# Kernel optimization log

Measured on AMD Instinct MI355X. Metric: run time of the kernel, lower is better.

The kernel has to match this reference:

```python
import jax, jax.numpy as jnp
import numpy as np

# ---- dims ----
N_NODES = 33      # nodes per graph (33-bus grid)
SEQ     = 24      # time steps per sample
BATCH   = 64      # samples
G       = BATCH * SEQ          # total graphs in the batch
EPG     = 64                   # directed edges per graph
E       = G * EPG              # total edges
N       = G * N_NODES          # total nodes
IN_CH   = 2
HID     = 64
HEADS   = 8
HC      = HID * HEADS          # 512
EDGE_DIM = 3
LSTM1_H = 128
LSTM2_H = 64
N_CLASSES = 4
NEG_SLOPE = 0.2


def setup_inputs() -> dict:
    key = jax.random.key(0)
    ks = jax.random.split(key, 32)
    rng = np.random.default_rng(0)

    # block-structured edge_index: every edge stays inside its own graph
    off = np.repeat(np.arange(G, dtype=np.int64) * N_NODES, EPG)
    src = rng.integers(0, N_NODES, E) + off
    dst = rng.integers(0, N_NODES, E) + off
    edge_index = jnp.asarray(np.stack([src, dst]), dtype=jnp.int32)

    def glorot(k, shape):
        fan = shape[0] + shape[-1]
        s = jnp.sqrt(6.0 / fan).astype(jnp.float32)
        return jax.random.uniform(k, shape, jnp.float32, -s, s)

    inp = dict(
        x=jax.random.normal(ks[0], (N, IN_CH), jnp.float32),
        edge_index=edge_index,
        edge_attr=jax.random.uniform(ks[1], (E, EDGE_DIM), jnp.float32),
        # GATv2 layer 1 (concat=True)
        g1_Wl=glorot(ks[2], (IN_CH, HC)),
        g1_Wr=glorot(ks[3], (IN_CH, HC)),
        g1_We=glorot(ks[4], (EDGE_DIM, HC)),
        g1_att=glorot(ks[5], (HEADS, HID)),
        g1_b=jnp.zeros((HC,), jnp.float32),
        # GATv2 layer 2 (concat=False -> head mean)
        g2_Wl=glorot(ks[6], (HC, HC)),
        g2_Wr=glorot(ks[7], (HC, HC)),
        g2_We=glorot(ks[8], (EDGE_DIM, HC)),
        g2_att=glorot(ks[9], (HEADS, HID)),
        g2_b=jnp.zeros((HID,), jnp.float32),
        # LSTM1: input 33*64=2112 -> 128, gates ordered (i,f,g,o)
        l1_Wih=0.05 * jax.random.normal(ks[10], (4 * LSTM1_H, N_NODES * HID), jnp.float32),
        l1_Whh=0.05 * jax.random.normal(ks[11], (4 * LSTM1_H, LSTM1_H), jnp.float32),
        l1_bih=jnp.zeros((4 * LSTM1_H,), jnp.float32),
        l1_bhh=jnp.zeros((4 * LSTM1_H,), jnp.float32),
        # LSTM2: 128 -> 64
        l2_Wih=0.05 * jax.random.normal(ks[12], (4 * LSTM2_H, LSTM1_H), jnp.float32),
        l2_Whh=0.05 * jax.random.normal(ks[13], (4 * LSTM2_H, LSTM2_H), jnp.float32),
        l2_bih=jnp.zeros((4 * LSTM2_H,), jnp.float32),
        l2_bhh=jnp.zeros((4 * LSTM2_H,), jnp.float32),
        # FC 64 -> n_classes
        fc_W=0.05 * jax.random.normal(ks[14], (N_CLASSES, LSTM2_H), jnp.float32),
        fc_b=jnp.zeros((N_CLASSES,), jnp.float32),
    )
    return inp


def _gatv2(x, edge_attr, src, dst, Wl, Wr, We, att, b, concat):
    """PyG GATv2Conv with edge_dim, add_self_loops semantics omitted is NOT used:
    we follow the message math: m = leaky_relu(xl[src]+xr[dst]+We@e),
    alpha = segment_softmax(<m,att>, dst), out = scatter_add(alpha * xl[src])."""
    n = x.shape[0]
    xl = (x @ Wl).reshape(n, HEADS, HID)      # [N,H,C]
    xr = (x @ Wr).reshape(n, HEADS, HID)
    em = (edge_attr @ We).reshape(-1, HEADS, HID)  # [E,H,C]
    m = jax.nn.leaky_relu(xl[src] + xr[dst] + em, NEG_SLOPE)
    logits = jnp.einsum('ehc,hc->eh', m, att)          # [E,H]
    mx = jax.ops.segment_max(logits, dst, num_segments=n)   # [N,H]
    ex = jnp.exp(logits - mx[dst])
    den = jax.ops.segment_sum(ex, dst, num_segments=n)
    alpha = ex / (den[dst] + 1e-16)                    # [E,H]
    out = jax.ops.segment_sum(xl[src] * alpha[:, :, None], dst, num_segments=n)  # [N,H,C]
    out = out.reshape(n, HC) if concat else out.mean(axis=1)
    return out + b


def _lstm(x, Wih, Whh, bih, bhh, hsz):
    B = x.shape[0]
    h0 = jnp.zeros((B, hsz), x.dtype)
    c0 = jnp.zeros((B, hsz), x.dtype)

    def step(carry, xt):
        h, c = carry
        gates = xt @ Wih.T + h @ Whh.T + bih + bhh
        i, f, g, o = jnp.split(gates, 4, axis=-1)
        i = jax.nn.sigmoid(i); f = jax.nn.sigmoid(f)
        g = jnp.tanh(g);       o = jax.nn.sigmoid(o)
        c = f * c + i * g
        h = o * jnp.tanh(c)
        return (h, c), h

    _, ys = jax.lax.scan(step, (h0, c0), x.transpose(1, 0, 2))  # [T,B,H]
    return ys.transpose(1, 0, 2)


def reference(x, edge_index, edge_attr,
              g1_Wl, g1_Wr, g1_We, g1_att, g1_b,
              g2_Wl, g2_Wr, g2_We, g2_att, g2_b,
              l1_Wih, l1_Whh, l1_bih, l1_bhh,
              l2_Wih, l2_Whh, l2_bih, l2_bhh,
              fc_W, fc_b):
    src, dst = edge_index[0], edge_index[1]
    h = jax.nn.elu(_gatv2(x, edge_attr, src, dst, g1_Wl, g1_Wr, g1_We, g1_att, g1_b, True))
    h = jax.nn.elu(_gatv2(h, edge_attr, src, dst, g2_Wl, g2_Wr, g2_We, g2_att, g2_b, False))
    seq = h.reshape(BATCH, SEQ, N_NODES * HID)          # [B,T,2112]
    seq = _lstm(seq, l1_Wih, l1_Whh, l1_bih, l1_bhh, LSTM1_H)
    seq = _lstm(seq, l2_Wih, l2_Whh, l2_bih, l2_bhh, LSTM2_H)
    last = seq[:, -1, :]                                 # [B,64]
    return last @ fc_W.T + fc_b                          # [B,n_classes]
```

## Files before the change

kernel.cpp:

```cpp
#include <hip/hip_runtime.h>
#include <math.h>

#define N_NODES 33
#define SEQ 24
#define BATCH 64
#define G_GRAPHS (BATCH * SEQ)
#define EPG 64
#define E_EDGES (G_GRAPHS * EPG)
#define N_TOTAL (G_GRAPHS * N_NODES)
#define HID 64
#define HEADS 8
#define HC (HID * HEADS)
#define LSTM1_H 128
#define LSTM2_H 64
#define NEG_SLOPE 0.2f
#define CONV_BLOCKS (128 + 264)

__device__ __forceinline__ float sigmoidf_(float x) { return 1.f / (1.f + expf(-x)); }
__device__ __forceinline__ float eluf_(float x) { return x > 0.f ? x : expm1f(x); }
__device__ __forceinline__ float lreluf_(float x) { return x > 0.f ? x : NEG_SLOPE * x; }

typedef __attribute__((ext_vector_type(4))) float f32x4;
typedef _Float16 half_t;
typedef __attribute__((ext_vector_type(8))) _Float16 halfx8;

__device__ __forceinline__ void gl2lds16(const void* g, void* l) {
  __builtin_amdgcn_global_load_lds(
      (__attribute__((address_space(1))) const unsigned int*)g,
      (__attribute__((address_space(3))) unsigned int*)l, 16, 0, 0);
}

__global__ __launch_bounds__(512) void gat1_kernel(
    const float* __restrict__ x, const int* __restrict__ src, const int* __restrict__ dst,
    const float* __restrict__ ea, const float* __restrict__ Wl, const float* __restrict__ Wr,
    const float* __restrict__ We, const float* __restrict__ att, const float* __restrict__ bias,
    half_t* __restrict__ h1, int g0, int gat_blocks,
    const float* __restrict__ g2Wl, const float* __restrict__ g2Wr,
    half_t* __restrict__ B2, const float* __restrict__ W1, half_t* __restrict__ W1f) {
  const int tid = threadIdx.x;

  __shared__ alignas(16) float Wl_s[2 * 512];
  __shared__ alignas(16) float Wr_s[2 * 512];
  __shared__ alignas(16) float We_s[3 * 512];
  __shared__ alignas(16) float att_s[512];
  __shared__ float xs0_s[N_NODES + 1], xs1_s[N_NODES + 1];
  __shared__ float easX[EPG], easY[EPG], easZ[EPG];
  __shared__ float logit_s[HEADS * 65];
  __shared__ int sloc[EPG], dloc[EPG], deg[N_NODES], start[N_NODES], fill[N_NODES], elist[EPG];
  __shared__ float tr[64 * 65];

  if ((int)blockIdx.x >= gat_blocks) {
    int cb = blockIdx.x - gat_blocks;
    if (cb < 128) {
      int kt = cb & 7, nt = cb >> 3;
      int k0 = kt * 64, n0 = nt * 64;
      int r = tid >> 6, c = tid & 63;
      #pragma unroll
      for (int rr = 0; rr < 8; ++rr) {
        int kl = rr * 8 + r;
        int n = n0 + c;
        float v = (n < 512) ? g2Wl[(size_t)(k0 + kl) * 512 + n]
                            : g2Wr[(size_t)(k0 + kl) * 512 + n - 512];
        tr[kl * 65 + c] = v;
      }
      __syncthreads();
      #pragma unroll
      for (int rr = 0; rr < 8; ++rr) {
        int nl = rr * 8 + r;
        B2[(size_t)(n0 + nl) * 512 + k0 + c] = (half_t)tr[c * 65 + nl];
      }
    } else {
      int base = (cb - 128) * 4096 + tid;
      #pragma unroll
      for (int i = 0; i < 8; ++i) {
        int idx = base + i * 512;
        if (idx < 512 * 2112) W1f[idx] = (half_t)W1[idx];
      }
    }
    return;
  }

  const int g = g0 + blockIdx.x;
  const int nb = g * N_NODES, eb = g * EPG;
  const int lb = blockIdx.x * N_NODES;

  for (int i = tid; i < 1024; i += 512) { Wl_s[i] = Wl[i]; Wr_s[i] = Wr[i]; }
  for (int i = tid; i < 1536; i += 512) We_s[i] = We[i];
  if (tid < 512) att_s[tid] = att[tid];
  if (tid < 2 * N_NODES) {
    float v = x[nb * 2 + tid];
    if (tid & 1) xs1_s[tid >> 1] = v; else xs0_s[tid >> 1] = v;
  }
  if (tid < EPG) {
    easX[tid] = ea[(eb + tid) * 3 + 0];
    easY[tid] = ea[(eb + tid) * 3 + 1];
    easZ[tid] = ea[(eb + tid) * 3 + 2];
    sloc[tid] = src[eb + tid] - nb;
    dloc[tid] = dst[eb + tid] - nb;
  }
  if (tid < N_NODES) { deg[tid] = 0; fill[tid] = 0; }
  __syncthreads();
  if (tid < EPG) atomicAdd(&deg[dloc[tid]], 1);
  __syncthreads();
  if (tid == 0) { int a = 0; for (int n = 0; n < N_NODES; ++n) { start[n] = a; a += deg[n]; } }
  __syncthreads();
  if (tid < EPG) { int d = dloc[tid]; int p = atomicAdd(&fill[d], 1); elist[start[d] + p] = tid; }

  {
    int h = tid >> 6, e = tid & 63;
    int s = sloc[e], d = dloc[e];
    float xs0 = xs0_s[s], xs1 = xs1_s[s], xd0 = xs0_s[d], xd1 = xs1_s[d];
    float e0 = easX[e], e1 = easY[e], e2 = easZ[e];
    float acc = 0.f;
    int base = h * 64;
    #pragma unroll
    for (int c4 = 0; c4 < 16; ++c4) {
      int j = base + c4 * 4;
      f32x4 wl0 = *(const f32x4*)(Wl_s + j);
      f32x4 wl1 = *(const f32x4*)(Wl_s + 512 + j);
      f32x4 wr0 = *(const f32x4*)(Wr_s + j);
      f32x4 wr1 = *(const f32x4*)(Wr_s + 512 + j);
      f32x4 we0 = *(const f32x4*)(We_s + j);
      f32x4 we1 = *(const f32x4*)(We_s + 512 + j);
      f32x4 we2 = *(const f32x4*)(We_s + 1024 + j);
      f32x4 at  = *(const f32x4*)(att_s + j);
      #pragma unroll
      for (int q = 0; q < 4; ++q) {
        float v = xs0 * wl0[q] + xs1 * wl1[q]
                + xd0 * wr0[q] + xd1 * wr1[q]
                + e0 * we0[q] + e1 * we1[q] + e2 * we2[q];
        acc += lreluf_(v) * at[q];
      }
    }
    logit_s[h * 65 + e] = acc;
  }
  __syncthreads();

  {
    int h = tid >> 6, n = tid & 63;
    if (n < N_NODES) {
      int s0 = start[n], dn = deg[n];
      float mx = -1e30f;
      for (int i = 0; i < dn; ++i) mx = fmaxf(mx, logit_s[h * 65 + elist[s0 + i]]);
      float den = 0.f;
      for (int i = 0; i < dn; ++i) den += expf(logit_s[h * 65 + elist[s0 + i]] - mx);
      float inv = 1.f / (den + 1e-16f);
      for (int i = 0; i < dn; ++i) {
        int e = elist[s0 + i];
        logit_s[h * 65 + e] = expf(logit_s[h * 65 + e] - mx) * inv;
      }
    }
  }
  __syncthreads();

  for (int t = tid; t < N_NODES * 64; t += 512) {
    int n = t >> 6, jb = t & 63;
    int j0 = jb * 8, h = jb >> 3;
    f32x4 wa0 = *(const f32x4*)(Wl_s + j0);
    f32x4 wa1 = *(const f32x4*)(Wl_s + j0 + 4);
    f32x4 wb0 = *(const f32x4*)(Wl_s + 512 + j0);
    f32x4 wb1 = *(const f32x4*)(Wl_s + 512 + j0 + 4);
    float acc[8] = {};
    int s0 = start[n], dn = deg[n];
    for (int i = 0; i < dn; ++i) {
      int e = elist[s0 + i]; int s = sloc[e];
      float a = logit_s[h * 65 + e];
      float ax0 = a * xs0_s[s], ax1 = a * xs1_s[s];
      #pragma unroll
      for (int q = 0; q < 4; ++q) {
        acc[q]     += ax0 * wa0[q] + ax1 * wb0[q];
        acc[4 + q] += ax0 * wa1[q] + ax1 * wb1[q];
      }
    }
    f32x4 b0 = *(const f32x4*)(bias + j0);
    f32x4 b1 = *(const f32x4*)(bias + j0 + 4);
    halfx8 vh;
    #pragma unroll
    for (int cc = 0; cc < 8; ++cc) {
      float bb = (cc < 4) ? b0[cc] : b1[cc - 4];
      vh[cc] = (half_t)eluf_(acc[cc] + bb);
    }
    *(halfx8*)(h1 + (size_t)(lb + n) * HC + j0) = vh;
  }
}

template <int WM, int WN, int NP, int K, int SA, int SB, typename TC>
__global__ __launch_bounds__(256) void gemm_f16(
    const half_t* __restrict__ A, const half_t* __restrict__ B,
    TC* __restrict__ C, const float* __restrict__ bias1, const float* __restrict__ bias2,
    int M, int N) {
  constexpr int BM = 32 * WM, BN = 32 * WN;
  constexpr bool BOUNCE = (sizeof(TC) == 2) && (BM == 128) && (BN == 128);
  constexpr int STAGE_HALFS = (BM + BN) * 32 * NP;
  constexpr int CT_HALFS = BOUNCE ? 128 * 132 : 0;
  constexpr int LDS_HALFS = STAGE_HALFS > CT_HALFS ? STAGE_HALFS : CT_HALFS;
  __shared__ half_t lds[LDS_HALFS];
  half_t* A_s = lds;
  half_t* B_s = A_s + NP * BM * 32;

  const int R = M / BM, NT = N / BN;
  int b = blockIdx.x;
  int xcd = b & 7, q = b >> 3;
  int ct = q % NT, rg = q / NT;
  int r = rg * 8 + xcd;
  if (r >= R) return;

  const int tid = threadIdx.x;
  const int wave = tid >> 6, lane = tid & 63;
  const int wm = wave >> 1, wn = wave & 1;
  const int bm = r * BM, bn = ct * BN;

  const int rA = lane >> 2;
  const int swz = (rA & 3) ^ ((rA >> 2) & 3);
  const int cA = ((lane & 3) ^ swz) * 8;

  f32x4 acc[WM][WN];
  #pragma unroll
  for (int tm = 0; tm < WM; ++tm)
    #pragma unroll
    for (int tn = 0; tn < WN; ++tn) acc[tm][tn] = {0.f, 0.f, 0.f, 0.f};

  for (int k0 = 0; k0 < K; k0 += 32 * NP) {
    #pragma unroll
    for (int p = 0; p < NP; ++p) {
      int kk = k0 + p * 32;
      #pragma unroll
      for (int i = 0; i < BM / 64; ++i) {
        int row = i * 64 + wave * 16;
        gl2lds16(A + (size_t)(bm + row + rA) * SA + kk + cA,
                 A_s + p * BM * 32 + row * 32);
      }
      #pragma unroll
      for (int i = 0; i < BN / 64; ++i) {
        int row = i * 64 + wave * 16;
        gl2lds16(B + (size_t)(bn + row + rA) * SB + kk + cA,
                 B_s + p * BN * 32 + row * 32);
      }
    }
    __syncthreads();

    const int fr = lane & 15;
    const int fs = (fr & 3) ^ ((fr >> 2) & 3);
    const int fk = ((lane >> 4) ^ fs) * 8;
    #pragma unroll
    for (int p = 0; p < NP; ++p) {
      const int pA = p * BM * 32, pB = p * BN * 32;
      halfx8 af[WM], bf[WN];
      #pragma unroll
      for (int tm = 0; tm < WM; ++tm) {
        int rr = (wm * WM + tm) * 16 + fr;
        af[tm] = *(const halfx8*)(A_s + pA + rr * 32 + fk);
      }
      #pragma unroll
      for (int tn = 0; tn < WN; ++tn) {
        int rr = (wn * WN + tn) * 16 + fr;
        bf[tn] = *(const halfx8*)(B_s + pB + rr * 32 + fk);
      }
      #pragma unroll
      for (int tm = 0; tm < WM; ++tm)
        #pragma unroll
        for (int tn = 0; tn < WN; ++tn)
          acc[tm][tn] = __builtin_amdgcn_mfma_f32_16x16x32_f16(af[tm], bf[tn], acc[tm][tn], 0, 0, 0);
    }
    __syncthreads();
  }

  const int col0 = lane & 15, rq = (lane >> 4) * 4;
  if constexpr (BOUNCE) {
    half_t* Cs = lds;
    #pragma unroll
    for (int tm = 0; tm < WM; ++tm)
      #pragma unroll
      for (int tn = 0; tn < WN; ++tn) {
        int cl = (wn * WN + tn) * 16 + col0;
        #pragma unroll
        for (int rr = 0; rr < 4; ++rr) {
          int rl = (wm * WM + tm) * 16 + rq + rr;
          Cs[rl * 132 + cl] = (half_t)acc[tm][tn][rr];
        }
      }
    __syncthreads();
    #pragma unroll
    for (int pass = 0; pass < 8; ++pass) {
      int row = pass * 16 + (tid >> 4);
      int col = (tid & 15) * 8;
      halfx8 v = *(const halfx8*)(Cs + row * 132 + col);
      *(halfx8*)((half_t*)C + (size_t)(bm + row) * N + bn + col) = v;
    }
  } else {
    #pragma unroll
    for (int tm = 0; tm < WM; ++tm)
      #pragma unroll
      for (int tn = 0; tn < WN; ++tn) {
        int col = bn + (wn * WN + tn) * 16 + col0;
        float badd = 0.f;
        if (bias1) badd += bias1[col];
        if (bias2) badd += bias2[col];
        #pragma unroll
        for (int rr = 0; rr < 4; ++rr) {
          int row = bm + (wm * WM + tm) * 16 + rq + rr;
          C[(size_t)row * N + col] = (TC)(acc[tm][tn][rr] + badd);
        }
      }
  }
}

__global__ __launch_bounds__(256) void gemm_f16_splitk(
    const half_t* __restrict__ A, const half_t* __restrict__ B,
    float* __restrict__ Cp, const float* __restrict__ bias1, const float* __restrict__ bias2,
    int M, int N) {
  constexpr int SA = 2112;
  __shared__ half_t lds[(64 + 64) * 64];
  half_t* A_s = lds;
  half_t* B_s = A_s + 2 * 64 * 32;

  const int part = blockIdx.y;
  const int koff = part ? 576 + (part - 1) * 512 : 0;
  const int kend = part ? 512 : 576;
  const half_t* Ap = A + koff;
  const half_t* Bp = B + koff;
  float* C = Cp + (size_t)part * M * N;

  const int R = M / 64, NT = N / 64;
  int b = blockIdx.x;
  int xcd = b & 7, q = b >> 3;
  int ct = q % NT, rg = q / NT;
  int r = rg * 8 + xcd;
  if (r >= R) return;

  const int tid = threadIdx.x;
  const int wave = tid >> 6, lane = tid & 63;
  const int wm = wave >> 1, wn = wave & 1;
  const int bm = r * 64, bn = ct * 64;

  const int rA = lane >> 2;
  const int swz = (rA & 3) ^ ((rA >> 2) & 3);
  const int cA = ((lane & 3) ^ swz) * 8;

  f32x4 acc[2][2];
  #pragma unroll
  for (int tm = 0; tm < 2; ++tm)
    #pragma unroll
    for (int tn = 0; tn < 2; ++tn) acc[tm][tn] = {0.f, 0.f, 0.f, 0.f};

  for (int k0 = 0; k0 < kend; k0 += 64) {
    #pragma unroll
    for (int p = 0; p < 2; ++p) {
      int kk = k0 + p * 32;
      int row = wave * 16;
      gl2lds16(Ap + (size_t)(bm + row + rA) * SA + kk + cA,
               A_s + p * 64 * 32 + row * 32);
      gl2lds16(Bp + (size_t)(bn + row + rA) * SA + kk + cA,
               B_s + p * 64 * 32 + row * 32);
    }
    __syncthreads();
    const int fr = lane & 15;
    const int fs = (fr & 3) ^ ((fr >> 2) & 3);
    const int fk = ((lane >> 4) ^ fs) * 8;
    #pragma unroll
    for (int p = 0; p < 2; ++p) {
      const int pA = p * 64 * 32, pB = p * 64 * 32;
      halfx8 af[2], bf[2];
      #pragma unroll
      for (int tm = 0; tm < 2; ++tm) {
        int rr = (wm * 2 + tm) * 16 + fr;
        af[tm] = *(const halfx8*)(A_s + pA + rr * 32 + fk);
      }
      #pragma unroll
      for (int tn = 0; tn < 2; ++tn) {
        int rr = (wn * 2 + tn) * 16 + fr;
        bf[tn] = *(const halfx8*)(B_s + pB + rr * 32 + fk);
      }
      #pragma unroll
      for (int tm = 0; tm < 2; ++tm)
        #pragma unroll
        for (int tn = 0; tn < 2; ++tn)
          acc[tm][tn] = __builtin_amdgcn_mfma_f32_16x16x32_f16(af[tm], bf[tn], acc[tm][tn], 0, 0, 0);
    }
    __syncthreads();
  }

  const int col0 = lane & 15, rq = (lane >> 4) * 4;
  #pragma unroll
  for (int tm = 0; tm < 2; ++tm)
    #pragma unroll
    for (int tn = 0; tn < 2; ++tn) {
      int col = bn + (wn * 2 + tn) * 16 + col0;
      float badd = (part == 0) ? (bias1[col] + bias2[col]) : 0.f;
      #pragma unroll
      for (int rr = 0; rr < 4; ++rr) {
        int row = bm + (wm * 2 + tm) * 16 + rq + rr;
        C[(size_t)row * N + col] = acc[tm][tn][rr] + badd;
      }
    }
}

__global__ __launch_bounds__(512) void gat2_kernel(
    const half_t* __restrict__ xlr, const int* __restrict__ src, const int* __restrict__ dst,
    const float* __restrict__ ea, const float* __restrict__ We,
    const float* __restrict__ att, const float* __restrict__ bias,
    half_t* __restrict__ h2, int g0) {
  __shared__ alignas(16) float We_s[3 * 512];
  __shared__ alignas(16) float att_s[512];
  __shared__ float b_s[HID];
  __shared__ float easX[EPG], easY[EPG], easZ[EPG];
  __shared__ float logit_s[HEADS * 65];
  __shared__ int sloc[EPG], dloc[EPG], deg[N_NODES], start[N_NODES], fill[N_NODES], elist[EPG];

  const int g = g0 + blockIdx.x, tid = threadIdx.x;
  const int nb = g * N_NODES, eb = g * EPG;
  const int lb = blockIdx.x * N_NODES;
  const int wave = tid >> 6, lane = tid & 63;

  for (int i = tid; i < 1536; i += 512) We_s[i] = We[i];
  if (tid < 512) att_s[tid] = att[tid];
  if (tid < HID) b_s[tid] = bias[tid];
  if (tid < EPG) {
    easX[tid] = ea[(eb + tid) * 3 + 0];
    easY[tid] = ea[(eb + tid) * 3 + 1];
    easZ[tid] = ea[(eb + tid) * 3 + 2];
    sloc[tid] = src[eb + tid] - nb;
    dloc[tid] = dst[eb + tid] - nb;
  }
  if (tid < N_NODES) { deg[tid] = 0; fill[tid] = 0; }
  __syncthreads();
  if (tid < EPG) atomicAdd(&deg[dloc[tid]], 1);
  __syncthreads();
  if (tid == 0) { int a = 0; for (int n = 0; n < N_NODES; ++n) { start[n] = a; a += deg[n]; } }
  __syncthreads();
  if (tid < EPG) { int d = dloc[tid]; int p = atomicAdd(&fill[d], 1); elist[start[d] + p] = tid; }
  __syncthreads();

  const int j0 = lane * 8;
  float w0[8], w1[8], w2[8], at8[8];
  #pragma unroll
  for (int q = 0; q < 8; ++q) {
    w0[q] = We_s[j0 + q];
    w1[q] = We_s[512 + j0 + q];
    w2[q] = We_s[1024 + j0 + q];
    at8[q] = att_s[j0 + q];
  }

  for (int e = wave; e < EPG; e += 8) {
    int s = sloc[e], d = dloc[e];
    halfx8 xlv = *((const halfx8*)(xlr + (size_t)(lb + s) * 1024) + lane);
    halfx8 xrv = *((const halfx8*)(xlr + (size_t)(lb + d) * 1024 + 512) + lane);
    float e0 = easX[e], e1 = easY[e], e2 = easZ[e];
    float acc = 0.f;
    #pragma unroll
    for (int q = 0; q < 8; ++q) {
      float v = (float)xlv[q] + (float)xrv[q] + e0 * w0[q] + e1 * w1[q] + e2 * w2[q];
      acc += lreluf_(v) * at8[q];
    }
    acc += __shfl_xor(acc, 1, 64);
    acc += __shfl_xor(acc, 2, 64);
    acc += __shfl_xor(acc, 4, 64);
    if ((lane & 7) == 0) logit_s[(lane >> 3) * 65 + e] = acc;
  }
  __syncthreads();

  {
    int h = tid >> 6, n = tid & 63;
    if (n < N_NODES) {
      int s0 = start[n], dn = deg[n];
      float mx = -1e30f;
      for (int i = 0; i < dn; ++i) mx = fmaxf(mx, logit_s[h * 65 + elist[s0 + i]]);
      float den = 0.f;
      for (int i = 0; i < dn; ++i) den += expf(logit_s[h * 65 + elist[s0 + i]] - mx);
      float inv = 1.f / (den + 1e-16f);
      for (int i = 0; i < dn; ++i) {
        int e = elist[s0 + i];
        logit_s[h * 65 + e] = expf(logit_s[h * 65 + e] - mx) * inv;
      }
    }
  }
  __syncthreads();

  for (int n = wave; n < N_NODES; n += 8) {
    float acc = 0.f;
    int s0 = start[n], dn = deg[n];
    for (int i = 0; i < dn; ++i) {
      int e = elist[s0 + i], s = sloc[e];
      const half_t* row = xlr + (size_t)(lb + s) * 1024 + lane;
      #pragma unroll
      for (int h = 0; h < 8; ++h)
        acc += logit_s[h * 65 + e] * (float)row[h * 64];
    }
    float v = eluf_(acc * 0.125f + b_s[lane]);
    h2[(size_t)(nb + n) * HID + lane] = (half_t)v;
  }
}

__global__ __launch_bounds__(1024, 4) void lstm_all(
    const float* __restrict__ X0, const float* __restrict__ X1,
    const float* __restrict__ X2p, const float* __restrict__ X3,
    const float* __restrict__ Whh1,
    const float* __restrict__ Wih2, const float* __restrict__ bih2,
    const float* __restrict__ bhh2, const float* __restrict__ Whh2,
    const float* __restrict__ fcW, const float* __restrict__ fcb,
    float* __restrict__ out) {
  __shared__ float hs1[LSTM1_H], cs1[LSTM1_H], p1[512], gs1[512];
  __shared__ float Y1s[SEQ][LSTM1_H];
  __shared__ float hs2[LSTM2_H], cs2[LSTM2_H], p2[4 * 256], gs2[256];
  const int tid = threadIdx.x, b = blockIdx.x;
  const int j = tid & 511, half = tid >> 9;

  float4 w1[16];
  {
    const float4* wp = (const float4*)(Whh1 + (size_t)j * LSTM1_H + half * 64);
    #pragma unroll
    for (int q = 0; q < 16; ++q) w1[q] = wp[q];
  }
  if (tid < LSTM1_H) { hs1[tid] = 0.f; cs1[tid] = 0.f; }
  __syncthreads();
  for (int t = 0; t < SEQ; ++t) {
    const float* hb = hs1 + half * 64;
    float acc = 0.f;
    #pragma unroll
    for (int q = 0; q < 16; ++q) {
      acc += w1[q].x * hb[4 * q] + w1[q].y * hb[4 * q + 1]
           + w1[q].z * hb[4 * q + 2] + w1[q].w * hb[4 * q + 3];
    }
    if (half) p1[j] = acc;
    __syncthreads();
    if (!half) {
      size_t xo = ((size_t)b * SEQ + t) * 512 + j;
      gs1[j] = acc + p1[j] + X0[xo] + X1[xo] + X2p[xo] + X3[xo];
    }
    __syncthreads();
    if (tid < LSTM1_H) {
      float ig = sigmoidf_(gs1[tid]);
      float fg = sigmoidf_(gs1[LSTM1_H + tid]);
      float gg = tanhf(gs1[2 * LSTM1_H + tid]);
      float og = sigmoidf_(gs1[3 * LSTM1_H + tid]);
      float c = fg * cs1[tid] + ig * gg;
      cs1[tid] = c;
      float h = og * tanhf(c);
      hs1[tid] = h;
      Y1s[t][tid] = h;
    }
    __syncthreads();
  }

  const int j2 = tid & 255, qt = tid >> 8;
  float4 w2x[8], w2h[4];
  {
    const float4* wxp = (const float4*)(Wih2 + (size_t)j2 * LSTM1_H + qt * 32);
    #pragma unroll
    for (int q = 0; q < 8; ++q) w2x[q] = wxp[q];
    const float4* whp = (const float4*)(Whh2 + (size_t)j2 * LSTM2_H + qt * 16);
    #pragma unroll
    for (int q = 0; q < 4; ++q) w2h[q] = whp[q];
  }
  if (tid < LSTM2_H) { hs2[tid] = 0.f; cs2[tid] = 0.f; }
  __syncthreads();
  for (int t = 0; t < SEQ; ++t) {
    const float* y = Y1s[t] + qt * 32;
    const float* hb = hs2 + qt * 16;
    float acc = 0.f;
    #pragma unroll
    for (int q = 0; q < 8; ++q) {
      acc += w2x[q].x * y[4 * q] + w2x[q].y * y[4 * q + 1]
           + w2x[q].z * y[4 * q + 2] + w2x[q].w * y[4 * q + 3];
    }
    #pragma unroll
    for (int q = 0; q < 4; ++q) {
      acc += w2h[q].x * hb[4 * q] + w2h[q].y * hb[4 * q + 1]
           + w2h[q].z * hb[4 * q + 2] + w2h[q].w * hb[4 * q + 3];
    }
    p2[qt * 256 + j2] = acc;
    __syncthreads();
    if (qt == 0)
      gs2[j2] = p2[j2] + p2[256 + j2] + p2[512 + j2] + p2[768 + j2]
              + bih2[j2] + bhh2[j2];
    __syncthreads();
    if (tid < LSTM2_H) {
      float ig = sigmoidf_(gs2[tid]);
      float fg = sigmoidf_(gs2[LSTM2_H + tid]);
      float gg = tanhf(gs2[2 * LSTM2_H + tid]);
      float og = sigmoidf_(gs2[3 * LSTM2_H + tid]);
      float c = fg * cs2[tid] + ig * gg;
      cs2[tid] = c;
      hs2[tid] = og * tanhf(c);
    }
    __syncthreads();
  }
  if (tid < 4) {
    float acc = fcb[tid];
    #pragma unroll
    for (int k = 0; k < LSTM2_H; ++k) acc += fcW[tid * LSTM2_H + k] * hs2[k];
    out[b * 4 + tid] = acc;
  }
}

extern "C" void kernel_launch(void* const* d_in, const int* in_sizes, int n_in,
                              void* d_out, int out_size, void* d_ws, size_t ws_size,
                              hipStream_t stream) {
  const float* x       = (const float*)d_in[0];
  const int*   eidx    = (const int*)d_in[1];
  const float* eattr   = (const float*)d_in[2];
  const float* g1_Wl   = (const float*)d_in[3];
  const float* g1_Wr   = (const float*)d_in[4];
  const float* g1_We   = (const float*)d_in[5];
  const float* g1_att  = (const float*)d_in[6];
  const float* g1_b    = (const float*)d_in[7];
  const float* g2_Wl   = (const float*)d_in[8];
  const float* g2_Wr   = (const float*)d_in[9];
  const float* g2_We   = (const float*)d_in[10];
  const float* g2_att  = (const float*)d_in[11];
  const float* g2_b    = (const float*)d_in[12];
  const float* l1_Wih  = (const float*)d_in[13];
  const float* l1_Whh  = (const float*)d_in[14];
  const float* l1_bih  = (const float*)d_in[15];
  const float* l1_bhh  = (const float*)d_in[16];
  const float* l2_Wih  = (const float*)d_in[17];
  const float* l2_Whh  = (const float*)d_in[18];
  const float* l2_bih  = (const float*)d_in[19];
  const float* l2_bhh  = (const float*)d_in[20];
  const float* fc_W    = (const float*)d_in[21];
  const float* fc_b    = (const float*)d_in[22];
  float* out = (float*)d_out;

  const int* src = eidx;
  const int* dst = eidx + E_EDGES;

  const int cand[5] = {1, 2, 3, 4, 6};
  int nchunks = 0;
  half_t *h1 = nullptr, *xlr2c = nullptr, *h2 = nullptr, *B2 = nullptr, *W1f = nullptr;
  float *X1p = nullptr;
  int chunk_g = 0, chunk_n = 0;
  for (int ci = 0; ci < 5; ++ci) {
    int C = cand[ci];
    int CG = G_GRAPHS / C, CN = CG * N_NODES;
    char* p = (char*)d_ws;
    auto alloc = [&](size_t bytes) { char* r = p; p += (bytes + 255) & ~(size_t)255; return r; };
    half_t* t_h1    = (half_t*)alloc((size_t)CN * HC * 2);
    half_t* t_xlr2c = (half_t*)alloc((size_t)CN * 1024 * 2);
    half_t* t_h2    = (half_t*)alloc((size_t)G_GRAPHS * 2112 * 2);
    half_t* t_B2    = (half_t*)alloc((size_t)1024 * 512 * 2);
    half_t* t_W1f   = (half_t*)alloc((size_t)512 * 2112 * 2);
    float*  t_X1p   = (float*)alloc((size_t)4 * G_GRAPHS * 512 * 4);
    if ((size_t)(p - (char*)d_ws) <= ws_size) {
      nchunks = C; chunk_g = CG; chunk_n = CN;
      h1 = t_h1; xlr2c = t_xlr2c; h2 = t_h2; B2 = t_B2; W1f = t_W1f;
      X1p = t_X1p;
      break;
    }
  }
  if (nchunks == 0) return;

  for (int c = 0; c < nchunks; ++c) {
    int g0 = c * chunk_g;
    int extra = (c == 0) ? CONV_BLOCKS : 0;
    gat1_kernel<<<chunk_g + extra, 512, 0, stream>>>(
        x, src, dst, eattr, g1_Wl, g1_Wr, g1_We, g1_att, g1_b, h1, g0, chunk_g,
        g2_Wl, g2_Wr, B2, l1_Wih, W1f);
    int R = chunk_n / 128, NT = 1024 / 128;
    int gblocks = 8 * ((R + 7) / 8) * NT;
    gemm_f16<4, 4, 2, HC, HC, HC, half_t><<<gblocks, 256, 0, stream>>>(
        h1, B2, xlr2c, (const float*)nullptr, (const float*)nullptr,
        chunk_n, 1024);
    gat2_kernel<<<chunk_g, 512, 0, stream>>>(xlr2c, src, dst, eattr, g2_We,
                                             g2_att, g2_b, h2, g0);
  }

  {
    dim3 grid(192, 4);
    gemm_f16_splitk<<<grid, 256, 0, stream>>>(h2, W1f, X1p, l1_bih, l1_bhh,
                                              G_GRAPHS, 512);
  }

  {
    size_t PS = (size_t)G_GRAPHS * 512;
    lstm_all<<<BATCH, 1024, 0, stream>>>(X1p, X1p + PS, X1p + 2 * PS, X1p + 3 * PS,
                                         l1_Whh, l2_Wih, l2_bih, l2_bhh, l2_Whh,
                                         fc_W, fc_b, out);
  }
}
```

Baseline: 344.7 us.

## Stage GAT2 node rows in LDS and drop a barrier per LSTM step

The GAT layer-2 kernel now copies each graph's 33 node rows (xl and xr halves) into shared memory with direct global-to-LDS loads. Edge logits and aggregation then read from LDS instead of re-gathering rows from global memory. Separately, both LSTM recurrences fold the partial-sum reduction into the gate-activation threads, removing one __syncthreads per time step, and the layer-2 bias is preloaded into a register. The staging adds about 66 KB of LDS per block, which lowers occupancy, and there is no visible wait or barrier between the async LDS copy and its first use.

```diff
diff --git a/kernel.cpp b/kernel.cpp
--- a/kernel.cpp
+++ b/kernel.cpp
@@ -400,6 +400,7 @@
     const float* __restrict__ ea, const float* __restrict__ We,
     const float* __restrict__ att, const float* __restrict__ bias,
     half_t* __restrict__ h2, int g0) {
+  __shared__ half_t x_s[N_NODES * 1024];
   __shared__ alignas(16) float We_s[3 * 512];
   __shared__ alignas(16) float att_s[512];
   __shared__ float b_s[HID];
@@ -411,6 +412,12 @@
   const int nb = g * N_NODES, eb = g * EPG;
   const int lb = blockIdx.x * N_NODES;
   const int wave = tid >> 6, lane = tid & 63;
+
+  for (int n = wave; n < N_NODES; n += 8) {
+    const half_t* grow = xlr + (size_t)(lb + n) * 1024;
+    gl2lds16(grow + lane * 8, x_s + n * 1024);
+    gl2lds16(grow + 512 + lane * 8, x_s + n * 1024 + 512);
+  }
 
   for (int i = tid; i < 1536; i += 512) We_s[i] = We[i];
   if (tid < 512) att_s[tid] = att[tid];
@@ -443,8 +450,8 @@
 
   for (int e = wave; e < EPG; e += 8) {
     int s = sloc[e], d = dloc[e];
-    halfx8 xlv = *((const halfx8*)(xlr + (size_t)(lb + s) * 1024) + lane);
-    halfx8 xrv = *((const halfx8*)(xlr + (size_t)(lb + d) * 1024 + 512) + lane);
+    halfx8 xlv = *((const halfx8*)(x_s + s * 1024) + lane);
+    halfx8 xrv = *((const halfx8*)(x_s + d * 1024 + 512) + lane);
     float e0 = easX[e], e1 = easY[e], e2 = easZ[e];
     float acc = 0.f;
     #pragma unroll
@@ -481,7 +488,7 @@
     int s0 = start[n], dn = deg[n];
     for (int i = 0; i < dn; ++i) {
       int e = elist[s0 + i], s = sloc[e];
-      const half_t* row = xlr + (size_t)(lb + s) * 1024 + lane;
+      const half_t* row = x_s + s * 1024 + lane;
       #pragma unroll
       for (int h = 0; h < 8; ++h)
         acc += logit_s[h * 65 + e] * (float)row[h * 64];
@@ -499,9 +506,9 @@
     const float* __restrict__ bhh2, const float* __restrict__ Whh2,
     const float* __restrict__ fcW, const float* __restrict__ fcb,
     float* __restrict__ out) {
-  __shared__ float hs1[LSTM1_H], cs1[LSTM1_H], p1[512], gs1[512];
+  __shared__ float hs1[LSTM1_H], cs1[LSTM1_H], p1[2][512];
   __shared__ float Y1s[SEQ][LSTM1_H];
-  __shared__ float hs2[LSTM2_H], cs2[LSTM2_H], p2[4 * 256], gs2[256];
+  __shared__ float hs2[LSTM2_H], cs2[LSTM2_H], p2[4][256];
   const int tid = threadIdx.x, b = blockIdx.x;
   const int j = tid & 511, half = tid >> 9;
 
@@ -521,19 +528,22 @@
       acc += w1[q].x * hb[4 * q] + w1[q].y * hb[4 * q + 1]
            + w1[q].z * hb[4 * q + 2] + w1[q].w * hb[4 * q + 3];
     }
-    if (half) p1[j] = acc;
-    __syncthreads();
     if (!half) {
       size_t xo = ((size_t)b * SEQ + t) * 512 + j;
-      gs1[j] = acc + p1[j] + X0[xo] + X1[xo] + X2p[xo] + X3[xo];
-    }
+      acc += X0[xo] + X1[xo] + X2p[xo] + X3[xo];
+    }
+    p1[half][j] = acc;
     __syncthreads();
     if (tid < LSTM1_H) {
-      float ig = sigmoidf_(gs1[tid]);
-      float fg = sigmoidf_(gs1[LSTM1_H + tid]);
-      float gg = tanhf(gs1[2 * LSTM1_H + tid]);
-      float og = sigmoidf_(gs1[3 * LSTM1_H + tid]);
-      float c = fg * cs1[tid] + ig * gg;
+      float gi = p1[0][tid] + p1[1][tid];
+      float gf = p1[0][LSTM1_H + tid] + p1[1][LSTM1_H + tid];
+      float gg = p1[0][2 * LSTM1_H + tid] + p1[1][2 * LSTM1_H + tid];
+      float go = p1[0][3 * LSTM1_H + tid] + p1[1][3 * LSTM1_H + tid];
+      float ig = sigmoidf_(gi);
+      float fg = sigmoidf_(gf);
+      float gv = tanhf(gg);
+      float og = sigmoidf_(go);
+      float c = fg * cs1[tid] + ig * gv;
       cs1[tid] = c;
       float h = og * tanhf(c);
       hs1[tid] = h;
@@ -544,6 +554,7 @@
 
   const int j2 = tid & 255, qt = tid >> 8;
   float4 w2x[8], w2h[4];
+  float bsum = 0.f;
   {
     const float4* wxp = (const float4*)(Wih2 + (size_t)j2 * LSTM1_H + qt * 32);
     #pragma unroll
@@ -551,13 +562,14 @@
     const float4* whp = (const float4*)(Whh2 + (size_t)j2 * LSTM2_H + qt * 16);
     #pragma unroll
     for (int q = 0; q < 4; ++q) w2h[q] = whp[q];
+    if (qt == 0) bsum = bih2[j2] + bhh2[j2];
   }
   if (tid < LSTM2_H) { hs2[tid] = 0.f; cs2[tid] = 0.f; }
   __syncthreads();
   for (int t = 0; t < SEQ; ++t) {
     const float* y = Y1s[t] + qt * 32;
     const float* hb = hs2 + qt * 16;
-    float acc = 0.f;
+    float acc = (qt == 0) ? bsum : 0.f;
     #pragma unroll
     for (int q = 0; q < 8; ++q) {
       acc += w2x[q].x * y[4 * q] + w2x[q].y * y[4 * q + 1]
@@ -568,18 +580,18 @@
       acc += w2h[q].x * hb[4 * q] + w2h[q].y * hb[4 * q + 1]
            + w2h[q].z * hb[4 * q + 2] + w2h[q].w * hb[4 * q + 3];
     }
-    p2[qt * 256 + j2] = acc;
-    __syncthreads();
-    if (qt == 0)
-      gs2[j2] = p2[j2] + p2[256 + j2] + p2[512 + j2] + p2[768 + j2]
-              + bih2[j2] + bhh2[j2];
+    p2[qt][j2] = acc;
     __syncthreads();
     if (tid < LSTM2_H) {
-      float ig = sigmoidf_(gs2[tid]);
-      float fg = sigmoidf_(gs2[LSTM2_H + tid]);
-      float gg = tanhf(gs2[2 * LSTM2_H + tid]);
-      float og = sigmoidf_(gs2[3 * LSTM2_H + tid]);
-      float c = fg * cs2[tid] + ig * gg;
+      float gi = p2[0][tid] + p2[1][tid] + p2[2][tid] + p2[3][tid];
+      float gf = p2[0][64 + tid] + p2[1][64 + tid] + p2[2][64 + tid] + p2[3][64 + tid];
+      float gg = p2[0][128 + tid] + p2[1][128 + tid] + p2[2][128 + tid] + p2[3][128 + tid];
+      float go = p2[0][192 + tid] + p2[1][192 + tid] + p2[2][192 + tid] + p2[3][192 + tid];
+      float ig = sigmoidf_(gi);
+      float fg = sigmoidf_(gf);
+      float gv = tanhf(gg);
+      float og = sigmoidf_(go);
+      float c = fg * cs2[tid] + ig * gv;
       cs2[tid] = c;
       hs2[tid] = og * tanhf(c);
     }
```

Result: no change. 350.7 us (+1.7%).
